# Kernel optimization log

Measured on AMD Instinct MI355X. Metric: run time of the kernel, lower is better.

Reference implementation:

```python
import jax, jax.numpy as jnp
import numpy as np

B, S, H = 2, 1024, 1024
N_IN, N_PROC = 512, 32


def _l2norm(x, eps=1e-12):
    n = jnp.linalg.norm(x, axis=-1, keepdims=True)
    return x / jnp.maximum(n, eps)


def setup_inputs() -> dict:
    key = jax.random.key(0)
    k1, k2, k3, k4 = jax.random.split(key, 4)
    intermediate = jax.random.normal(k1, (B, S, H), dtype=jnp.float32)
    input_activations = jax.random.normal(k2, (B, S, N_IN), dtype=jnp.float32)
    # params (torch defaults: pattern_templates ~ randn; Linear weight ~ U scaled)
    pattern_templates = jax.random.normal(k3, (N_PROC, N_IN), dtype=jnp.float32)
    bound = 1.0 / np.sqrt(H)
    W_transform = jax.random.uniform(k4, (N_PROC * H, H), dtype=jnp.float32,
                                     minval=-bound, maxval=bound)
    return {"intermediate": intermediate, "input_activations": input_activations,
            "pattern_templates": pattern_templates, "W_transform": W_transform}


def reference(intermediate, input_activations, pattern_templates, W_transform):
    # pattern matching -> soft routing weights  [B,S,N_proc]
    act_norm = _l2norm(input_activations)
    tmpl_norm = _l2norm(pattern_templates)
    process_activations = jax.nn.sigmoid(
        jnp.einsum('bsi,ni->bsn', act_norm, tmpl_norm))
    # dispatch: weighted sum over sequence (batched GEMM instead of bcast-mul-sum)
    contexts = jnp.einsum('bsh,bsn->bnh', intermediate, process_activations)
    norm = process_activations.sum(axis=1)[..., None] + 1e-8  # [B,N_proc,1]
    contexts = contexts / norm
    # per-process-neuron HxH transform (torch Linear weight is [out,in])
    Wn = W_transform.reshape(N_PROC, H, H)  # [n, k(out), h(in)]
    transformed = jnp.einsum('bnh,nkh->bnk', contexts, Wn)
    # combine back to tokens  [B,S,H]
    combined = jnp.einsum('bnh,bsn->bsh', transformed, process_activations)
    return combined, process_activations
```

## Files before the change

kernel.cpp:

```cpp
#include <hip/hip_runtime.h>
#include <math.h>

#define B 2
#define S 1024
#define H 1024
#define NIN 512
#define NP 32
#define SC 16
#define SCHUNK (S / SC)

__global__ __launch_bounds__(256)
void k_pattern(const float* __restrict__ act, const float* __restrict__ tmpl,
               float* __restrict__ P, float* __restrict__ nrm) {
    __shared__ float act_lds[8][NIN];
    __shared__ float invn[NP];
    __shared__ float psum[8][NP];
    int tid = threadIdx.x;
    int t0 = blockIdx.x * 8;
    int b  = t0 >> 10;

    {
        const float4* src = (const float4*)(act + (size_t)t0 * NIN);
        float4* dst = (float4*)(&act_lds[0][0]);
        for (int k = tid; k < 8 * NIN / 4; k += 256) dst[k] = src[k];
    }
    {
        int n = tid >> 3, s8 = tid & 7;
        const float* tr = tmpl + (size_t)n * NIN;
        float ss = 0.f;
#pragma unroll 16
        for (int k = 0; k < 64; ++k) { float x = tr[s8 + 8 * k]; ss += x * x; }
        ss += __shfl_xor(ss, 1); ss += __shfl_xor(ss, 2); ss += __shfl_xor(ss, 4);
        if (s8 == 0) invn[n] = 1.f / fmaxf(sqrtf(ss), 1e-12f);
    }
    __syncthreads();

    int tok = tid >> 5;
    int sub = tid & 31;
    float ss = 0.f;
#pragma unroll
    for (int k = 0; k < 16; ++k) { float x = act_lds[tok][sub + 32 * k]; ss += x * x; }
#pragma unroll
    for (int m = 16; m; m >>= 1) ss += __shfl_xor(ss, m);
    float inva = 1.f / fmaxf(sqrtf(ss), 1e-12f);

    float4 av[4];
#pragma unroll
    for (int q = 0; q < 4; ++q)
        av[q] = *(const float4*)(&act_lds[tok][sub * 4 + q * 128]);

    float dot[NP];
#pragma unroll
    for (int n = 0; n < NP; ++n) {
        const float* tr = tmpl + (size_t)n * NIN + sub * 4;
        float d = 0.f;
#pragma unroll
        for (int q = 0; q < 4; ++q) {
            float4 tv = *(const float4*)(tr + q * 128);
            d += tv.x * av[q].x + tv.y * av[q].y + tv.z * av[q].z + tv.w * av[q].w;
        }
        dot[n] = d;
    }
    float myd = 0.f;
#pragma unroll
    for (int n = 0; n < NP; ++n) {
        float d = dot[n];
        d += __shfl_xor(d, 1); d += __shfl_xor(d, 2); d += __shfl_xor(d, 4);
        d += __shfl_xor(d, 8); d += __shfl_xor(d, 16);
        if (sub == n) myd = d;
    }
    float p = 1.f / (1.f + expf(-myd * inva * invn[sub]));
    P[(size_t)(t0 + tok) * NP + sub] = p;
    psum[tok][sub] = p;
    __syncthreads();
    if (tid < NP) {
        float s = 0.f;
#pragma unroll
        for (int t = 0; t < 8; ++t) s += psum[t][tid];
        unsafeAtomicAdd(&nrm[b * NP + tid], s);
    }
}

__global__ __launch_bounds__(256)
void k_ctx_partial(const float* __restrict__ I, const float* __restrict__ P,
                   float* __restrict__ part) {
    int bid = blockIdx.x;
    int ht = bid & 7;
    int sc = (bid >> 3) & (SC - 1);
    int b  = bid >> 7;
    int tid = threadIdx.x;
    int hl = tid & 127;
    int g  = __builtin_amdgcn_readfirstlane(tid >> 7);
    int h  = ht * 128 + hl;
    int s0 = sc * SCHUNK;
    const float* Pb = P + ((size_t)b * S + s0) * NP + g * 16;
    const float* Ip = I + ((size_t)b * S + s0) * H + h;
    float acc[16];
#pragma unroll
    for (int j = 0; j < 16; ++j) acc[j] = 0.f;
#pragma unroll 4
    for (int s = 0; s < SCHUNK; ++s) {
        float x = Ip[(size_t)s * H];
#pragma unroll
        for (int j = 0; j < 16; ++j) acc[j] += x * Pb[s * NP + j];
    }
    size_t base = (((size_t)b * SC + sc) * NP + g * 16) * H + h;
#pragma unroll
    for (int j = 0; j < 16; ++j) part[base + (size_t)j * H] = acc[j];
}

__global__ __launch_bounds__(256)
void k_ctx_reduce(const float* __restrict__ part, float* __restrict__ ctx) {
    int idx = blockIdx.x * 256 + threadIdx.x;
    int b = idx >> 15;
    int rem = idx & 32767;
    float s = 0.f;
#pragma unroll
    for (int sc = 0; sc < SC; ++sc)
        s += part[((size_t)b * SC + sc) * (NP * H) + rem];
    ctx[idx] = s;
}

__global__ __launch_bounds__(256, 4)
void k_transform(const float* __restrict__ W, const float* __restrict__ ctx,
                 const float* __restrict__ nrm, float* __restrict__ T) {
    int bid = blockIdx.x;
    int n  = bid >> 6;
    int rg = bid & 63;
    int tid = threadIdx.x;
    int w = tid >> 6, lane = tid & 63;

    float inv0 = 1.f / (nrm[n] + 1e-8f);
    float inv1 = 1.f / (nrm[NP + n] + 1e-8f);

    const float4* c0g = (const float4*)(ctx + (size_t)n * H);
    const float4* c1g = (const float4*)(ctx + ((size_t)NP + n) * H);
    float4 c0[4], c1[4];
#pragma unroll
    for (int it = 0; it < 4; ++it) {
        float4 v = c0g[it * 64 + lane];
        c0[it] = make_float4(v.x * inv0, v.y * inv0, v.z * inv0, v.w * inv0);
        float4 u = c1g[it * 64 + lane];
        c1[it] = make_float4(u.x * inv1, u.y * inv1, u.z * inv1, u.w * inv1);
    }

    int row0 = rg * 16 + w * 4;
    const float4* Wr = (const float4*)(W + ((size_t)n * H + row0) * H);
    float a0[4] = {0.f, 0.f, 0.f, 0.f};
    float a1[4] = {0.f, 0.f, 0.f, 0.f};
#pragma unroll
    for (int it = 0; it < 4; ++it) {
#pragma unroll
        for (int r = 0; r < 4; ++r) {
            float4 wv = Wr[r * 256 + it * 64 + lane];
            a0[r] += wv.x * c0[it].x + wv.y * c0[it].y + wv.z * c0[it].z + wv.w * c0[it].w;
            a1[r] += wv.x * c1[it].x + wv.y * c1[it].y + wv.z * c1[it].z + wv.w * c1[it].w;
        }
    }
#pragma unroll
    for (int r = 0; r < 4; ++r) {
#pragma unroll
        for (int off = 32; off; off >>= 1) {
            a0[r] += __shfl_xor(a0[r], off);
            a1[r] += __shfl_xor(a1[r], off);
        }
    }
    if (lane == 0) {
#pragma unroll
        for (int r = 0; r < 4; ++r) {
            T[(size_t)n * H + row0 + r] = a0[r];
            T[((size_t)NP + n) * H + row0 + r] = a1[r];
        }
    }
}

__global__ __launch_bounds__(256)
void k_combine(const float* __restrict__ T, const float* __restrict__ P,
               float* __restrict__ out) {
    int bid = blockIdx.x;
    int ht = bid & 3;
    int sc = (bid >> 2) & 63;
    int b  = bid >> 8;
    int tid = threadIdx.x;
    __shared__ float Tl[NP][256];
    int h0 = ht * 256;
    for (int k = tid; k < NP * 256; k += 256) {
        int n = k >> 8, h = k & 255;
        Tl[n][h] = T[((size_t)b * NP + n) * H + h0 + h];
    }
    __syncthreads();
    int s0 = sc * 16;
    const float* Pb = P + ((size_t)b * S + s0) * NP;
    float acc[16];
#pragma unroll
    for (int s = 0; s < 16; ++s) acc[s] = 0.f;
#pragma unroll
    for (int n0 = 0; n0 < NP; n0 += 4) {
        float t0v = Tl[n0 + 0][tid];
        float t1v = Tl[n0 + 1][tid];
        float t2v = Tl[n0 + 2][tid];
        float t3v = Tl[n0 + 3][tid];
#pragma unroll
        for (int s = 0; s < 16; ++s) {
            const float* pr = Pb + s * NP + n0;
            acc[s] += t0v * pr[0] + t1v * pr[1] + t2v * pr[2] + t3v * pr[3];
        }
    }
#pragma unroll
    for (int s = 0; s < 16; ++s)
        out[((size_t)b * S + s0 + s) * H + h0 + tid] = acc[s];
}

extern "C" void kernel_launch(void* const* d_in, const int* in_sizes, int n_in,
                              void* d_out, int out_size, void* d_ws, size_t ws_size,
                              hipStream_t stream) {
    const float* I    = (const float*)d_in[0];
    const float* act  = (const float*)d_in[1];
    const float* tmpl = (const float*)d_in[2];
    const float* W    = (const float*)d_in[3];
    float* out  = (float*)d_out;
    float* Pout = out + (size_t)B * S * H;

    float* ws   = (float*)d_ws;
    float* nrm  = ws;
    float* part = nrm + 64;
    float* ctx  = part + (size_t)B * SC * NP * H;
    float* T    = ctx + (size_t)B * NP * H;

    hipMemsetAsync(nrm, 0, (size_t)B * NP * sizeof(float), stream);
    k_pattern    <<<B * S / 8,            256, 0, stream>>>(act, tmpl, Pout, nrm);
    k_ctx_partial<<<B * SC * 8,           256, 0, stream>>>(I, Pout, part);
    k_ctx_reduce <<<B * NP * H / 256,     256, 0, stream>>>(part, ctx);
    k_transform  <<<NP * 64,              256, 0, stream>>>(W, ctx, nrm, T);
    k_combine    <<<B * 64 * 4,           256, 0, stream>>>(T, Pout, out);
}
```

Measured before the change: 81.37 us.

## Fuse all five stages into one persistent kernel with software grid barriers

Replaces the five separate launches with a single persistent kernel of 256 blocks that runs each stage in turn, separated by an atomic-counter grid barrier. The aim is to remove the per-launch overhead and the idle gaps between stages. The atomic accumulation of normalisers is replaced by recomputing the column sums of P inside the transform stage, and the P reads become float4 vector loads. In exchange, only 256 blocks are in flight, which may underuse the GPU during the bandwidth-heavy W stage. The barrier also relies on every block being resident at the same time.

```diff
diff --git a/kernel.cpp b/kernel.cpp
--- a/kernel.cpp
+++ b/kernel.cpp
@@ -7,208 +7,218 @@
 #define NIN 512
 #define NP 32
 #define SC 16
-#define SCHUNK (S / SC)
-
-__global__ __launch_bounds__(256)
-void k_pattern(const float* __restrict__ act, const float* __restrict__ tmpl,
-               float* __restrict__ P, float* __restrict__ nrm) {
-    __shared__ float act_lds[8][NIN];
-    __shared__ float invn[NP];
-    __shared__ float psum[8][NP];
-    int tid = threadIdx.x;
-    int t0 = blockIdx.x * 8;
-    int b  = t0 >> 10;
-
-    {
+#define SCHUNK 64
+#define NBLK 256
+#define NTHR 256
+
+__device__ __forceinline__ void grid_sync(unsigned* cnt, unsigned* gen) {
+    __syncthreads();
+    if (threadIdx.x == 0) {
+        unsigned g = __hip_atomic_load(gen, __ATOMIC_RELAXED, __HIP_MEMORY_SCOPE_AGENT);
+        unsigned old = __hip_atomic_fetch_add(cnt, 1u, __ATOMIC_ACQ_REL, __HIP_MEMORY_SCOPE_AGENT);
+        if (old == NBLK - 1u) {
+            __hip_atomic_store(cnt, 0u, __ATOMIC_RELAXED, __HIP_MEMORY_SCOPE_AGENT);
+            __hip_atomic_fetch_add(gen, 1u, __ATOMIC_RELEASE, __HIP_MEMORY_SCOPE_AGENT);
+        } else {
+            while (__hip_atomic_load(gen, __ATOMIC_ACQUIRE, __HIP_MEMORY_SCOPE_AGENT) == g)
+                __builtin_amdgcn_s_sleep(2);
+        }
+    }
+    __syncthreads();
+}
+
+__global__ __launch_bounds__(NTHR)
+void k_fused(const float* __restrict__ I, const float* __restrict__ act,
+             const float* __restrict__ tmpl, const float* __restrict__ W,
+             float* __restrict__ out, float* __restrict__ P,
+             float* __restrict__ part, float* __restrict__ ctx, float* __restrict__ T,
+             unsigned* cnt, unsigned* gen) {
+    __shared__ float lds[NP * 256];
+    const int tid = threadIdx.x;
+    const int bid = blockIdx.x;
+
+    {
+        int t0 = bid * 8;
         const float4* src = (const float4*)(act + (size_t)t0 * NIN);
-        float4* dst = (float4*)(&act_lds[0][0]);
-        for (int k = tid; k < 8 * NIN / 4; k += 256) dst[k] = src[k];
-    }
-    {
-        int n = tid >> 3, s8 = tid & 7;
-        const float* tr = tmpl + (size_t)n * NIN;
+        float4* dst = (float4*)lds;
+        for (int k = tid; k < 8 * NIN / 4; k += NTHR) dst[k] = src[k];
+        {
+            int n = tid >> 3, s8 = tid & 7;
+            const float* tr = tmpl + (size_t)n * NIN;
+            float ss = 0.f;
+#pragma unroll 16
+            for (int k = 0; k < 64; ++k) { float x = tr[s8 + 8 * k]; ss += x * x; }
+            ss += __shfl_xor(ss, 1); ss += __shfl_xor(ss, 2); ss += __shfl_xor(ss, 4);
+            if (s8 == 0) lds[4096 + n] = 1.f / fmaxf(sqrtf(ss), 1e-12f);
+        }
+        __syncthreads();
+        int tok = tid >> 5, sub = tid & 31;
+        const float* arow = lds + tok * NIN;
         float ss = 0.f;
-#pragma unroll 16
-        for (int k = 0; k < 64; ++k) { float x = tr[s8 + 8 * k]; ss += x * x; }
-        ss += __shfl_xor(ss, 1); ss += __shfl_xor(ss, 2); ss += __shfl_xor(ss, 4);
-        if (s8 == 0) invn[n] = 1.f / fmaxf(sqrtf(ss), 1e-12f);
-    }
-    __syncthreads();
-
-    int tok = tid >> 5;
-    int sub = tid & 31;
-    float ss = 0.f;
-#pragma unroll
-    for (int k = 0; k < 16; ++k) { float x = act_lds[tok][sub + 32 * k]; ss += x * x; }
-#pragma unroll
-    for (int m = 16; m; m >>= 1) ss += __shfl_xor(ss, m);
-    float inva = 1.f / fmaxf(sqrtf(ss), 1e-12f);
-
-    float4 av[4];
-#pragma unroll
-    for (int q = 0; q < 4; ++q)
-        av[q] = *(const float4*)(&act_lds[tok][sub * 4 + q * 128]);
-
-    float dot[NP];
-#pragma unroll
-    for (int n = 0; n < NP; ++n) {
-        const float* tr = tmpl + (size_t)n * NIN + sub * 4;
-        float d = 0.f;
-#pragma unroll
-        for (int q = 0; q < 4; ++q) {
-            float4 tv = *(const float4*)(tr + q * 128);
-            d += tv.x * av[q].x + tv.y * av[q].y + tv.z * av[q].z + tv.w * av[q].w;
-        }
-        dot[n] = d;
-    }
-    float myd = 0.f;
-#pragma unroll
-    for (int n = 0; n < NP; ++n) {
-        float d = dot[n];
-        d += __shfl_xor(d, 1); d += __shfl_xor(d, 2); d += __shfl_xor(d, 4);
-        d += __shfl_xor(d, 8); d += __shfl_xor(d, 16);
-        if (sub == n) myd = d;
-    }
-    float p = 1.f / (1.f + expf(-myd * inva * invn[sub]));
-    P[(size_t)(t0 + tok) * NP + sub] = p;
-    psum[tok][sub] = p;
-    __syncthreads();
-    if (tid < NP) {
-        float s = 0.f;
-#pragma unroll
-        for (int t = 0; t < 8; ++t) s += psum[t][tid];
-        unsafeAtomicAdd(&nrm[b * NP + tid], s);
-    }
-}
-
-__global__ __launch_bounds__(256)
-void k_ctx_partial(const float* __restrict__ I, const float* __restrict__ P,
-                   float* __restrict__ part) {
-    int bid = blockIdx.x;
-    int ht = bid & 7;
-    int sc = (bid >> 3) & (SC - 1);
-    int b  = bid >> 7;
-    int tid = threadIdx.x;
-    int hl = tid & 127;
-    int g  = __builtin_amdgcn_readfirstlane(tid >> 7);
-    int h  = ht * 128 + hl;
-    int s0 = sc * SCHUNK;
-    const float* Pb = P + ((size_t)b * S + s0) * NP + g * 16;
-    const float* Ip = I + ((size_t)b * S + s0) * H + h;
-    float acc[16];
-#pragma unroll
-    for (int j = 0; j < 16; ++j) acc[j] = 0.f;
-#pragma unroll 4
-    for (int s = 0; s < SCHUNK; ++s) {
-        float x = Ip[(size_t)s * H];
-#pragma unroll
-        for (int j = 0; j < 16; ++j) acc[j] += x * Pb[s * NP + j];
-    }
-    size_t base = (((size_t)b * SC + sc) * NP + g * 16) * H + h;
-#pragma unroll
-    for (int j = 0; j < 16; ++j) part[base + (size_t)j * H] = acc[j];
-}
-
-__global__ __launch_bounds__(256)
-void k_ctx_reduce(const float* __restrict__ part, float* __restrict__ ctx) {
-    int idx = blockIdx.x * 256 + threadIdx.x;
-    int b = idx >> 15;
-    int rem = idx & 32767;
-    float s = 0.f;
-#pragma unroll
-    for (int sc = 0; sc < SC; ++sc)
-        s += part[((size_t)b * SC + sc) * (NP * H) + rem];
-    ctx[idx] = s;
-}
-
-__global__ __launch_bounds__(256, 4)
-void k_transform(const float* __restrict__ W, const float* __restrict__ ctx,
-                 const float* __restrict__ nrm, float* __restrict__ T) {
-    int bid = blockIdx.x;
-    int n  = bid >> 6;
-    int rg = bid & 63;
-    int tid = threadIdx.x;
-    int w = tid >> 6, lane = tid & 63;
-
-    float inv0 = 1.f / (nrm[n] + 1e-8f);
-    float inv1 = 1.f / (nrm[NP + n] + 1e-8f);
-
-    const float4* c0g = (const float4*)(ctx + (size_t)n * H);
-    const float4* c1g = (const float4*)(ctx + ((size_t)NP + n) * H);
-    float4 c0[4], c1[4];
-#pragma unroll
-    for (int it = 0; it < 4; ++it) {
-        float4 v = c0g[it * 64 + lane];
-        c0[it] = make_float4(v.x * inv0, v.y * inv0, v.z * inv0, v.w * inv0);
-        float4 u = c1g[it * 64 + lane];
-        c1[it] = make_float4(u.x * inv1, u.y * inv1, u.z * inv1, u.w * inv1);
-    }
-
-    int row0 = rg * 16 + w * 4;
-    const float4* Wr = (const float4*)(W + ((size_t)n * H + row0) * H);
-    float a0[4] = {0.f, 0.f, 0.f, 0.f};
-    float a1[4] = {0.f, 0.f, 0.f, 0.f};
-#pragma unroll
-    for (int it = 0; it < 4; ++it) {
-#pragma unroll
-        for (int r = 0; r < 4; ++r) {
-            float4 wv = Wr[r * 256 + it * 64 + lane];
-            a0[r] += wv.x * c0[it].x + wv.y * c0[it].y + wv.z * c0[it].z + wv.w * c0[it].w;
-            a1[r] += wv.x * c1[it].x + wv.y * c1[it].y + wv.z * c1[it].z + wv.w * c1[it].w;
-        }
-    }
-#pragma unroll
-    for (int r = 0; r < 4; ++r) {
-#pragma unroll
-        for (int off = 32; off; off >>= 1) {
-            a0[r] += __shfl_xor(a0[r], off);
-            a1[r] += __shfl_xor(a1[r], off);
-        }
-    }
-    if (lane == 0) {
-#pragma unroll
-        for (int r = 0; r < 4; ++r) {
-            T[(size_t)n * H + row0 + r] = a0[r];
-            T[((size_t)NP + n) * H + row0 + r] = a1[r];
-        }
-    }
-}
-
-__global__ __launch_bounds__(256)
-void k_combine(const float* __restrict__ T, const float* __restrict__ P,
-               float* __restrict__ out) {
-    int bid = blockIdx.x;
-    int ht = bid & 3;
-    int sc = (bid >> 2) & 63;
-    int b  = bid >> 8;
-    int tid = threadIdx.x;
-    __shared__ float Tl[NP][256];
-    int h0 = ht * 256;
-    for (int k = tid; k < NP * 256; k += 256) {
-        int n = k >> 8, h = k & 255;
-        Tl[n][h] = T[((size_t)b * NP + n) * H + h0 + h];
-    }
-    __syncthreads();
-    int s0 = sc * 16;
-    const float* Pb = P + ((size_t)b * S + s0) * NP;
-    float acc[16];
-#pragma unroll
-    for (int s = 0; s < 16; ++s) acc[s] = 0.f;
-#pragma unroll
-    for (int n0 = 0; n0 < NP; n0 += 4) {
-        float t0v = Tl[n0 + 0][tid];
-        float t1v = Tl[n0 + 1][tid];
-        float t2v = Tl[n0 + 2][tid];
-        float t3v = Tl[n0 + 3][tid];
-#pragma unroll
-        for (int s = 0; s < 16; ++s) {
-            const float* pr = Pb + s * NP + n0;
-            acc[s] += t0v * pr[0] + t1v * pr[1] + t2v * pr[2] + t3v * pr[3];
-        }
-    }
-#pragma unroll
-    for (int s = 0; s < 16; ++s)
-        out[((size_t)b * S + s0 + s) * H + h0 + tid] = acc[s];
+#pragma unroll
+        for (int k = 0; k < 16; ++k) { float x = arow[sub + 32 * k]; ss += x * x; }
+#pragma unroll
+        for (int m = 16; m; m >>= 1) ss += __shfl_xor(ss, m);
+        float inva = 1.f / fmaxf(sqrtf(ss), 1e-12f);
+        float4 av[4];
+#pragma unroll
+        for (int q = 0; q < 4; ++q) av[q] = *(const float4*)(arow + sub * 4 + q * 128);
+        float myd = 0.f;
+#pragma unroll
+        for (int n = 0; n < NP; ++n) {
+            const float* trp = tmpl + (size_t)n * NIN + sub * 4;
+            float d = 0.f;
+#pragma unroll
+            for (int q = 0; q < 4; ++q) {
+                float4 tv = *(const float4*)(trp + q * 128);
+                d += tv.x * av[q].x + tv.y * av[q].y + tv.z * av[q].z + tv.w * av[q].w;
+            }
+            d += __shfl_xor(d, 1); d += __shfl_xor(d, 2); d += __shfl_xor(d, 4);
+            d += __shfl_xor(d, 8); d += __shfl_xor(d, 16);
+            if (sub == n) myd = d;
+        }
+        float p = 1.f / (1.f + expf(-myd * inva * lds[4096 + sub]));
+        P[(size_t)(t0 + tok) * NP + sub] = p;
+    }
+    grid_sync(cnt, gen);
+
+    {
+        int ht = bid & 7, sc = (bid >> 3) & 15, b = bid >> 7;
+        int hl = tid & 127;
+        int g16 = (tid >> 7) * 16;
+        int goff = g16;
+        asm volatile("" : "+v"(goff));
+        int h = ht * 128 + hl;
+        int s0 = sc * SCHUNK;
+        const float* Pb = P + ((size_t)b * S + s0) * NP + goff;
+        const float* Ip = I + ((size_t)b * S + s0) * H + h;
+        float acc[16];
+#pragma unroll
+        for (int j = 0; j < 16; ++j) acc[j] = 0.f;
+#pragma unroll 2
+        for (int s = 0; s < SCHUNK; ++s) {
+            float x = Ip[(size_t)s * H];
+            float4 pv[4];
+#pragma unroll
+            for (int q = 0; q < 4; ++q) pv[q] = *(const float4*)(Pb + s * NP + 4 * q);
+#pragma unroll
+            for (int q = 0; q < 4; ++q) {
+                acc[4*q+0] += x * pv[q].x; acc[4*q+1] += x * pv[q].y;
+                acc[4*q+2] += x * pv[q].z; acc[4*q+3] += x * pv[q].w;
+            }
+        }
+        size_t base = (((size_t)b * SC + sc) * NP + g16) * H + h;
+#pragma unroll
+        for (int j = 0; j < 16; ++j) part[base + (size_t)j * H] = acc[j];
+    }
+    grid_sync(cnt, gen);
+
+    {
+        int idx = bid * NTHR + tid;
+        int b = idx >> 15, rem = idx & 32767;
+        float ssum = 0.f;
+#pragma unroll
+        for (int sc = 0; sc < SC; ++sc)
+            ssum += part[((size_t)b * SC + sc) * (NP * H) + rem];
+        ctx[idx] = ssum;
+    }
+    grid_sync(cnt, gen);
+
+    {
+        int n = bid >> 3, rg8 = bid & 7;
+        int bb = tid >> 7, j = tid & 127;
+        int pj = j;
+        asm volatile("" : "+v"(pj));
+        float ps = 0.f;
+#pragma unroll
+        for (int m = 0; m < 8; ++m)
+            ps += P[((size_t)bb * S + pj + 128 * m) * NP + n];
+        lds[tid] = ps;
+        __syncthreads();
+#pragma unroll
+        for (int off = 64; off >= 1; off >>= 1) {
+            if (j < off) lds[tid] += lds[tid + off];
+            __syncthreads();
+        }
+        float inv0 = 1.f / (lds[0] + 1e-8f);
+        float inv1 = 1.f / (lds[128] + 1e-8f);
+        int w = tid >> 6, lane = tid & 63;
+        const float4* c0g = (const float4*)(ctx + (size_t)n * H);
+        const float4* c1g = (const float4*)(ctx + ((size_t)NP + n) * H);
+        float4 c0[4], c1[4];
+#pragma unroll
+        for (int it = 0; it < 4; ++it) {
+            float4 v = c0g[it * 64 + lane];
+            c0[it] = make_float4(v.x * inv0, v.y * inv0, v.z * inv0, v.w * inv0);
+            float4 u = c1g[it * 64 + lane];
+            c1[it] = make_float4(u.x * inv1, u.y * inv1, u.z * inv1, u.w * inv1);
+        }
+        for (int rg = 0; rg < 8; ++rg) {
+            int row0 = rg8 * 128 + rg * 16 + w * 4;
+            const float4* Wr = (const float4*)(W + ((size_t)n * H + row0) * H);
+            float a0[4] = {0.f,0.f,0.f,0.f}, a1[4] = {0.f,0.f,0.f,0.f};
+#pragma unroll
+            for (int it = 0; it < 4; ++it) {
+#pragma unroll
+                for (int r = 0; r < 4; ++r) {
+                    float4 wv = Wr[r * 256 + it * 64 + lane];
+                    a0[r] += wv.x*c0[it].x + wv.y*c0[it].y + wv.z*c0[it].z + wv.w*c0[it].w;
+                    a1[r] += wv.x*c1[it].x + wv.y*c1[it].y + wv.z*c1[it].z + wv.w*c1[it].w;
+                }
+            }
+#pragma unroll
+            for (int r = 0; r < 4; ++r) {
+#pragma unroll
+                for (int off = 32; off; off >>= 1) {
+                    a0[r] += __shfl_xor(a0[r], off);
+                    a1[r] += __shfl_xor(a1[r], off);
+                }
+            }
+            if (lane == 0) {
+#pragma unroll
+                for (int r = 0; r < 4; ++r) {
+                    T[(size_t)n * H + row0 + r] = a0[r];
+                    T[((size_t)NP + n) * H + row0 + r] = a1[r];
+                }
+            }
+        }
+    }
+    grid_sync(cnt, gen);
+
+    {
+        int b = bid >> 7, ht = (bid >> 5) & 3, sc2 = bid & 31;
+        int h0 = ht * 256;
+        for (int k = tid; k < NP * 256; k += NTHR) {
+            int n = k >> 8, h = k & 255;
+            lds[k] = T[((size_t)b * NP + n) * H + h0 + h];
+        }
+        __syncthreads();
+        unsigned poff = 0;
+        asm volatile("" : "+v"(poff));
+#pragma unroll
+        for (int u = 0; u < 2; ++u) {
+            int s0 = (sc2 * 2 + u) * 16;
+            const float4* P4 = (const float4*)(P + ((size_t)b * S + s0) * NP + poff);
+            float acc[16];
+#pragma unroll
+            for (int s = 0; s < 16; ++s) acc[s] = 0.f;
+#pragma unroll
+            for (int n0 = 0; n0 < NP; n0 += 4) {
+                float t0v = lds[(n0 + 0) * 256 + tid];
+                float t1v = lds[(n0 + 1) * 256 + tid];
+                float t2v = lds[(n0 + 2) * 256 + tid];
+                float t3v = lds[(n0 + 3) * 256 + tid];
+#pragma unroll
+                for (int s = 0; s < 16; ++s) {
+                    float4 pv = P4[s * 8 + n0 / 4];
+                    acc[s] += t0v * pv.x + t1v * pv.y + t2v * pv.z + t3v * pv.w;
+                }
+            }
+#pragma unroll
+            for (int s = 0; s < 16; ++s)
+                out[((size_t)b * S + s0 + s) * H + h0 + tid] = acc[s];
+        }
+    }
 }
 
 extern "C" void kernel_launch(void* const* d_in, const int* in_sizes, int n_in,
@@ -221,16 +231,13 @@
     float* out  = (float*)d_out;
     float* Pout = out + (size_t)B * S * H;
 
-    float* ws   = (float*)d_ws;
-    float* nrm  = ws;
-    float* part = nrm + 64;
+    unsigned* cnt = (unsigned*)d_ws;
+    float* fws  = (float*)d_ws;
+    float* part = fws + 16;
     float* ctx  = part + (size_t)B * SC * NP * H;
     float* T    = ctx + (size_t)B * NP * H;
 
-    hipMemsetAsync(nrm, 0, (size_t)B * NP * sizeof(float), stream);
-    k_pattern    <<<B * S / 8,            256, 0, stream>>>(act, tmpl, Pout, nrm);
-    k_ctx_partial<<<B * SC * 8,           256, 0, stream>>>(I, Pout, part);
-    k_ctx_reduce <<<B * NP * H / 256,     256, 0, stream>>>(part, ctx);
-    k_transform  <<<NP * 64,              256, 0, stream>>>(W, ctx, nrm, T);
-    k_combine    <<<B * 64 * 4,           256, 0, stream>>>(T, Pout, out);
+    hipMemsetAsync(d_ws, 0, 2 * sizeof(unsigned), stream);
+    k_fused<<<NBLK, NTHR, 0, stream>>>(I, act, tmpl, W, out, Pout, part, ctx, T,
+                                       cnt, cnt + 1);
 }
```

Result: slower. 196.9 us (+142.0%).
